# Performance work log

Hardware: AMD Instinct MI355X
Metric: run time of the kernel (lower is better)

Reference implementation:

```python
import jax, jax.numpy as jnp
from jax import lax
import numpy as np

D_COND = 48      # d_condition
K = 24           # n_bins
HID = 128        # hidden_dim
T = 10           # n_transforms
TAIL = 15.0      # tail_bound
B = 131072       # batch (contexts x samples flattened, as in sample())


def setup_inputs() -> dict:
    key = jax.random.key(0)
    ks = jax.random.split(key, 8)
    def w(k, shape, fan_in, gain=1.0):
        return (jax.random.normal(k, shape, jnp.float32) * (gain / np.sqrt(fan_in))).astype(jnp.float32)
    return {
        "z": jax.random.normal(ks[0], (B,), jnp.float32),
        "context": jax.random.normal(ks[1], (B, D_COND), jnp.float32),
        "W0": w(ks[2], (T, D_COND, HID), D_COND),
        "b0": jnp.zeros((T, HID), jnp.float32),
        "W1": w(ks[3], (T, HID, HID), HID),
        "b1": jnp.zeros((T, HID), jnp.float32),
        "W2": w(ks[4], (T, HID, HID), HID),
        "b2": jnp.zeros((T, HID), jnp.float32),
        "W3": w(ks[5], (T, HID, 3 * K + 1), HID, gain=0.1),
        "b3": jnp.zeros((T, 3 * K + 1), jnp.float32),
        "loc": jnp.float32(85.0),
        "scale": jnp.float32(5.0),
    }


def _spline_forward(x, widths, heights, derivs):
    # x: (B,); widths/heights: (B,K); derivs: (B,K+1)
    inside = (x >= -TAIL) & (x <= TAIL)
    cw = jnp.pad(jnp.cumsum(widths, -1), ((0, 0), (1, 0)), constant_values=-TAIL)   # (B,K+1)
    ch = jnp.pad(jnp.cumsum(heights, -1), ((0, 0), (1, 0)), constant_values=-TAIL)  # (B,K+1)
    # torch.searchsorted(cw[...,1:], x, right=False) == count of elems < x
    idx = jnp.clip(jnp.sum(cw[:, 1:] < x[:, None], axis=-1), 0, K - 1)
    take = lambda a, i: jnp.take_along_axis(a, i[:, None], axis=-1)[:, 0]
    w_k = take(widths, idx)
    h_k = take(heights, idx)
    cw_k = take(cw, idx)
    ch_k = take(ch, idx)
    d_k = take(derivs, idx)
    d_k1 = take(derivs, idx + 1)
    s = h_k / w_k
    xi = jnp.clip((x - cw_k) / w_k, 1e-6, 1.0 - 1e-6)
    one_m = 1.0 - xi
    numer = h_k * (s * xi * xi + d_k * xi * one_m)
    denom = s + (d_k + d_k1 - 2.0 * s) * xi * one_m
    y = ch_k + numer / denom
    dy_dxi = s * s * (d_k1 * xi * xi + 2.0 * s * xi * one_m + d_k * one_m * one_m) / (denom * denom)
    log_det = (jnp.log(jnp.maximum(dy_dxi, 1e-10))
               + jnp.log(jnp.maximum(h_k, 1e-10))
               - jnp.log(jnp.maximum(w_k, 1e-10)))
    y = jnp.where(inside, y, x)
    log_det = jnp.where(inside, log_det, 0.0)
    return y, log_det


def reference(z, context, W0, b0, W1, b1, W2, b2, W3, b3, loc, scale):
    def body(carry, p):
        zc, ld = carry
        w0, c0, w1, c1, w2, c2, w3, c3 = p
        h = jax.nn.silu(context @ w0 + c0)
        h = jax.nn.silu(h @ w1 + c1)
        h = jax.nn.silu(h @ w2 + c2)
        params = h @ w3 + c3                                   # (B, 3K+1)
        Wl, Hl, Dl = params[:, :K], params[:, K:2 * K], params[:, 2 * K:]
        widths = jax.nn.softmax(Wl, axis=-1) * (2.0 * TAIL)
        heights = jax.nn.softmax(Hl, axis=-1) * (2.0 * TAIL)
        derivs = jax.nn.softplus(Dl) + 1e-3
        y, l = _spline_forward(zc, widths, heights, derivs)
        return (y, ld + l), None

    (z_out, total_ld), _ = lax.scan(body, (z, jnp.zeros_like(z)),
                                    (W0, b0, W1, b1, W2, b2, W3, b3))
    s = jnp.maximum(scale, 0.1)
    temp_f = z_out * s + loc   # _unstandardize, as in sample()
    return temp_f, total_ld
```

## Files before the change

kernel.cpp:

```cpp
#include <hip/hip_runtime.h>
#include <hip/hip_bf16.h>

#define DCOND 48
#define KBINS 24
#define HID 128
#define TSTEPS 10
#define NPAR 73
#define TAILF 15.0f

typedef __attribute__((ext_vector_type(8))) short v8s;
typedef __attribute__((ext_vector_type(4))) float f32x4;
typedef __attribute__((ext_vector_type(4))) unsigned u32x4;

__device__ __forceinline__ short f2bf(float f) {
    __hip_bfloat16 h = __float2bfloat16(f);
    return __builtin_bit_cast(short, h);
}
__device__ __forceinline__ float bf2f(short s) {
    unsigned u = ((unsigned)(unsigned short)s) << 16;
    return __builtin_bit_cast(float, u);
}
__device__ __forceinline__ float silu_f(float v) {
    return __fdividef(v, 1.0f + __expf(-v));
}

__device__ __forceinline__ unsigned cvt_pk(float a, float b) {
    unsigned r;
    asm("v_cvt_pk_bf16_f32 %0, %1, %2" : "=v"(r) : "v"(a), "v"(b));
    return r;
}

__device__ __forceinline__ void split8(f32x4 a0, f32x4 a1, v8s& hi, v8s& lo) {
    unsigned h0 = cvt_pk(a0[0], a0[1]);
    unsigned h1 = cvt_pk(a0[2], a0[3]);
    unsigned h2 = cvt_pk(a1[0], a1[1]);
    unsigned h3 = cvt_pk(a1[2], a1[3]);
    float l0 = a0[0] - __builtin_bit_cast(float, h0 << 16);
    float l1 = a0[1] - __builtin_bit_cast(float, h0 & 0xffff0000u);
    float l2 = a0[2] - __builtin_bit_cast(float, h1 << 16);
    float l3 = a0[3] - __builtin_bit_cast(float, h1 & 0xffff0000u);
    float l4 = a1[0] - __builtin_bit_cast(float, h2 << 16);
    float l5 = a1[1] - __builtin_bit_cast(float, h2 & 0xffff0000u);
    float l6 = a1[2] - __builtin_bit_cast(float, h3 << 16);
    float l7 = a1[3] - __builtin_bit_cast(float, h3 & 0xffff0000u);
    unsigned q0 = cvt_pk(l0, l1);
    unsigned q1 = cvt_pk(l2, l3);
    unsigned q2 = cvt_pk(l4, l5);
    unsigned q3 = cvt_pk(l6, l7);
    hi = __builtin_bit_cast(v8s, (u32x4){h0, h1, h2, h3});
    lo = __builtin_bit_cast(v8s, (u32x4){q0, q1, q2, q3});
}

__global__ void prep_w(const float* __restrict__ W0, const float* __restrict__ W1,
                       const float* __restrict__ W2, const float* __restrict__ W3,
                       short* __restrict__ ws)
{
    int g = blockIdx.x * 256 + threadIdx.x;
    if (g >= TSTEPS * 51200) return;
    int t = g / 51200;
    int r = g % 51200;

    int base_e, elems, NT, Kreal, Nreal;
    const float* W;
    if (r < 8192)       { base_e = 0;     elems = 8192;  NT = 8; Kreal = 48;  Nreal = 128; W = W0 + (size_t)t * DCOND * HID; }
    else if (r < 24576) { base_e = 8192;  elems = 16384; NT = 8; Kreal = 128; Nreal = 128; W = W1 + (size_t)t * HID * HID; }
    else if (r < 40960) { base_e = 24576; elems = 16384; NT = 8; Kreal = 128; Nreal = 128; W = W2 + (size_t)t * HID * HID; }
    else                { base_e = 40960; elems = 10240; NT = 5; Kreal = 128; Nreal = 73;  W = W3 + (size_t)t * HID * NPAR; }

    int e  = r - base_e;
    int j  = e & 7;
    int ln = (e >> 3) & 63;
    int q  = e >> 9;
    int nt = q % NT, kc = q / NT;
    int k  = kc * 32 + (ln >> 4) * 8 + j;
    int n  = nt * 16 + (ln & 15);

    float v = 0.0f;
    if (k < Kreal && n < Nreal) v = W[(size_t)k * Nreal + n];
    short hi = f2bf(v);
    short lo = f2bf(v - bf2f(hi));

    size_t o = (size_t)t * 102400 + 2 * (size_t)base_e + e;
    ws[o]         = hi;
    ws[o + elems] = lo;
}

#define MBLK 128
#define NTHR 512

template<int ROUNDS>
__device__ __forceinline__ void w_issue(const short* __restrict__ g, int tid, v8s (&r)[8]) {
    #pragma unroll
    for (int i = 0; i < ROUNDS; ++i)
        r[i] = *(const v8s*)(g + tid * 8 + i * 4096);
}
template<int ROUNDS>
__device__ __forceinline__ void w_flush(short* __restrict__ lds, int tid, const v8s (&r)[8]) {
    #pragma unroll
    for (int i = 0; i < ROUNDS; ++i)
        *(v8s*)(lds + tid * 8 + i * 4096) = r[i];
}

template<int KC, int NT, int ELEMS, bool ACT, bool AREG>
__device__ __forceinline__ void layer_run(const float* __restrict__ bias, int nreal,
                                          float* __restrict__ Hlds,
                                          const short* __restrict__ Wb,
                                          int lane, int wave,
                                          const v8s* cxh, const v8s* cxl)
{
    const int arow = wave * 16 + (lane & 15);
    const int asw  = (arow & 7) << 4;
    const int kg   = (lane >> 4) * 8;

    v8s ah[KC], al[KC];
    if (AREG) {
        #pragma unroll
        for (int kc = 0; kc < KC; ++kc) { ah[kc] = cxh[kc]; al[kc] = cxl[kc]; }
    } else {
        #pragma unroll
        for (int kc = 0; kc < KC; ++kc) {
            const int kb = (kc * 32 + kg) * 4;
            f32x4 a0 = *(const f32x4*)((const char*)Hlds + arow * 512 + (kb ^ asw));
            f32x4 a1 = *(const f32x4*)((const char*)Hlds + arow * 512 + ((kb + 16) ^ asw));
            split8(a0, a1, ah[kc], al[kc]);
        }
    }

    const int crow0 = wave * 16 + (lane >> 4) * 4;
    const int ncol  = lane & 15;

    #pragma unroll
    for (int np = 0; np < NT / 2; ++np) {
        const int nt0 = np * 2, nt1 = np * 2 + 1;
        const int n0 = nt0 * 16 + ncol, n1 = nt1 * 16 + ncol;
        const float bv0 = (n0 < nreal) ? bias[n0] : 0.0f;
        const float bv1 = (n1 < nreal) ? bias[n1] : 0.0f;
        f32x4 acc0 = {bv0, bv0, bv0, bv0};
        f32x4 acc1 = {bv1, bv1, bv1, bv1};
        #pragma unroll
        for (int kc = 0; kc < KC; ++kc) {
            const short* bp0 = Wb + ((size_t)(kc * NT + nt0) * 64 + lane) * 8;
            const short* bp1 = Wb + ((size_t)(kc * NT + nt1) * 64 + lane) * 8;
            v8s bh0 = *(const v8s*)bp0;
            v8s bl0 = *(const v8s*)(bp0 + ELEMS);
            v8s bh1 = *(const v8s*)bp1;
            v8s bl1 = *(const v8s*)(bp1 + ELEMS);
            acc0 = __builtin_amdgcn_mfma_f32_16x16x32_bf16(ah[kc], bh0, acc0, 0, 0, 0);
            acc1 = __builtin_amdgcn_mfma_f32_16x16x32_bf16(ah[kc], bh1, acc1, 0, 0, 0);
            acc0 = __builtin_amdgcn_mfma_f32_16x16x32_bf16(ah[kc], bl0, acc0, 0, 0, 0);
            acc1 = __builtin_amdgcn_mfma_f32_16x16x32_bf16(ah[kc], bl1, acc1, 0, 0, 0);
            acc0 = __builtin_amdgcn_mfma_f32_16x16x32_bf16(al[kc], bh0, acc0, 0, 0, 0);
            acc1 = __builtin_amdgcn_mfma_f32_16x16x32_bf16(al[kc], bh1, acc1, 0, 0, 0);
        }
        #pragma unroll
        for (int r = 0; r < 4; ++r) {
            const int row = crow0 + r;
            const int sw  = (row & 7) << 4;
            float v0 = acc0[r], v1 = acc1[r];
            if (ACT) { v0 = silu_f(v0); v1 = silu_f(v1); }
            *(float*)((char*)Hlds + row * 512 + ((n0 * 4) ^ sw)) = v0;
            *(float*)((char*)Hlds + row * 512 + ((n1 * 4) ^ sw)) = v1;
        }
    }
    if (NT & 1) {
        const int nt = NT - 1;
        const int n0 = nt * 16 + ncol;
        const float bv0 = (n0 < nreal) ? bias[n0] : 0.0f;
        f32x4 acc0 = {bv0, bv0, bv0, bv0};
        #pragma unroll
        for (int kc = 0; kc < KC; ++kc) {
            const short* bp0 = Wb + ((size_t)(kc * NT + nt) * 64 + lane) * 8;
            v8s bh0 = *(const v8s*)bp0;
            v8s bl0 = *(const v8s*)(bp0 + ELEMS);
            acc0 = __builtin_amdgcn_mfma_f32_16x16x32_bf16(ah[kc], bh0, acc0, 0, 0, 0);
            acc0 = __builtin_amdgcn_mfma_f32_16x16x32_bf16(ah[kc], bl0, acc0, 0, 0, 0);
            acc0 = __builtin_amdgcn_mfma_f32_16x16x32_bf16(al[kc], bh0, acc0, 0, 0, 0);
        }
        #pragma unroll
        for (int r = 0; r < 4; ++r) {
            const int row = crow0 + r;
            const int sw  = (row & 7) << 4;
            float v0 = acc0[r];
            if (ACT) v0 = silu_f(v0);
            *(float*)((char*)Hlds + row * 512 + ((n0 * 4) ^ sw)) = v0;
        }
    }
}

__global__ __launch_bounds__(NTHR, 2)
void nsf_mfma(const float* __restrict__ z_g, const float* __restrict__ ctx_g,
              const float* __restrict__ b0g, const float* __restrict__ b1g,
              const float* __restrict__ b2g, const float* __restrict__ b3g,
              const float* __restrict__ locp, const float* __restrict__ sclp,
              const short* __restrict__ wsW, float* __restrict__ out, int B)
{
    __shared__ float Hlds[MBLK * 128];
    __shared__ short Wlds[32768];
    const int tid  = threadIdx.x;
    const int lane = tid & 63, wave = tid >> 6;
    const int blk  = blockIdx.x;

    v8s wreg[8];
    w_issue<4>(wsW, tid, wreg);

    v8s cxh[2], cxl[2];
    {
        const int arow = wave * 16 + (lane & 15);
        int gidr = blk * MBLK + arow;
        if (gidr > B - 1) gidr = B - 1;
        const int k0 = (lane >> 4) * 8;
        const float* cg = ctx_g + (size_t)gidr * DCOND;
        f32x4 c0 = *(const f32x4*)(cg + k0);
        f32x4 c1 = *(const f32x4*)(cg + k0 + 4);
        split8(c0, c1, cxh[0], cxl[0]);
        if ((lane >> 4) < 2) {
            f32x4 c2 = *(const f32x4*)(cg + 32 + k0);
            f32x4 c3 = *(const f32x4*)(cg + 36 + k0);
            split8(c2, c3, cxh[1], cxl[1]);
        } else {
            #pragma unroll
            for (int u = 0; u < 8; ++u) { cxh[1][u] = 0; cxl[1][u] = 0; }
        }
    }

    float x = 0.0f, ld = 0.0f;
    if (lane < 16) {
        int gid = blk * MBLK + wave * 16 + lane;
        if (gid > B - 1) gid = B - 1;
        x = z_g[gid];
    }

    #pragma unroll 1
    for (int t = 0; t < TSTEPS; ++t) {
        const short* wstep = wsW + (size_t)t * 102400;
        const short* wnext = wsW + (size_t)((t + 1) % TSTEPS) * 102400;

        w_flush<4>(Wlds, tid, wreg);
        w_issue<8>(wstep + 16384, tid, wreg);
        __syncthreads();

        layer_run<2, 8, 8192, true, true>(b0g + t * HID, HID, Hlds, Wlds,
                                          lane, wave, cxh, cxl);
        __syncthreads();

        w_flush<8>(Wlds, tid, wreg);
        w_issue<8>(wstep + 49152, tid, wreg);
        __syncthreads();

        layer_run<4, 8, 16384, true, false>(b1g + t * HID, HID, Hlds, Wlds,
                                            lane, wave, nullptr, nullptr);
        __syncthreads();

        w_flush<8>(Wlds, tid, wreg);
        w_issue<5>(wstep + 81920, tid, wreg);
        __syncthreads();

        layer_run<4, 8, 16384, true, false>(b2g + t * HID, HID, Hlds, Wlds,
                                            lane, wave, nullptr, nullptr);
        __syncthreads();

        w_flush<5>(Wlds, tid, wreg);
        w_issue<4>(wnext, tid, wreg);
        __syncthreads();

        layer_run<4, 5, 10240, false, false>(b3g + t * NPAR, NPAR, Hlds, Wlds,
                                             lane, wave, nullptr, nullptr);

        if (lane < 16) {
            const int rowS = wave * 16 + lane;
            const char* hrow = (const char*)Hlds + rowS * 512;
            const int sw = (rowS & 7) << 4;

            float pw[KBINS], ph[KBINS];
            #pragma unroll
            for (int g = 0; g < 6; ++g) {
                f32x4 vw = *(const f32x4*)(hrow + ((g * 16) ^ sw));
                f32x4 vh = *(const f32x4*)(hrow + (((g + 6) * 16) ^ sw));
                #pragma unroll
                for (int u = 0; u < 4; ++u) { pw[g * 4 + u] = vw[u]; ph[g * 4 + u] = vh[u]; }
            }
            float mw = pw[0], mh = ph[0];
            #pragma unroll
            for (int i = 1; i < KBINS; ++i) { mw = fmaxf(mw, pw[i]); mh = fmaxf(mh, ph[i]); }
            float wsum = 0.0f, hsum = 0.0f;
            #pragma unroll
            for (int i = 0; i < KBINS; ++i) {
                pw[i] = __expf(pw[i] - mw); wsum += pw[i];
                ph[i] = __expf(ph[i] - mh); hsum += ph[i];
            }
            const float wmul = __fdividef(2.0f * TAILF, wsum);
            const float hmul = __fdividef(2.0f * TAILF, hsum);

            float cw = 0.0f, ch = 0.0f;
            float cwk = -TAILF, chk = -TAILF;
            float wk = pw[0] * wmul, hk = ph[0] * hmul;
            int idx = 0;
            #pragma unroll
            for (int i = 1; i < KBINS; ++i) {
                cw += pw[i - 1] * wmul;
                ch += ph[i - 1] * hmul;
                if (cw < x) {
                    cwk = cw; chk = ch;
                    wk = pw[i] * wmul; hk = ph[i] * hmul;
                    idx = i;
                }
            }
            float d0 = *(const float*)(hrow + (((2 * KBINS + idx) * 4) ^ sw));
            float d1 = *(const float*)(hrow + (((2 * KBINS + idx + 1) * 4) ^ sw));
            const float dk  = fmaxf(d0, 0.0f) + __logf(1.0f + __expf(-fabsf(d0))) + 0.001f;
            const float dk1 = fmaxf(d1, 0.0f) + __logf(1.0f + __expf(-fabsf(d1))) + 0.001f;

            const bool inside = (x >= -TAILF) && (x <= TAILF);
            const float sr = __fdividef(hk, wk);
            float xi = __fdividef(x - cwk, wk);
            xi = fminf(fmaxf(xi, 1e-6f), 1.0f - 1e-6f);
            const float om  = 1.0f - xi;
            const float xio = xi * om;
            const float numer = hk * (sr * xi * xi + dk * xio);
            const float denom = sr + (dk + dk1 - 2.0f * sr) * xio;
            const float y = chk + __fdividef(numer, denom);
            const float dyd = __fdividef(sr * sr * (dk1 * xi * xi + 2.0f * sr * xio + dk * om * om),
                                         denom * denom);
            const float lg = __logf(fmaxf(dyd, 1e-10f)) + __logf(fmaxf(hk, 1e-10f))
                           - __logf(fmaxf(wk, 1e-10f));
            x  = inside ? y : x;
            ld += inside ? lg : 0.0f;
        }
        __syncthreads();
    }

    if (lane < 16) {
        const int gid = blk * MBLK + wave * 16 + lane;
        if (gid < B) {
            const float s = fmaxf(sclp[0], 0.1f);
            out[gid]     = fmaf(x, s, locp[0]);
            out[B + gid] = ld;
        }
    }
}

#define FBLK 256
template<int KIN, int WS, int NOUT, bool ACT>
__device__ __forceinline__ void dense_chunk(const float* __restrict__ W,
                                            const float* __restrict__ bias,
                                            int j0, const float (&hin)[KIN],
                                            float* __restrict__ sb, int tid)
{
    #pragma unroll 1
    for (int jj = 0; jj < NOUT; jj += 8) {
        const int j = j0 + jj;
        float a[8];
        #pragma unroll
        for (int u = 0; u < 8; ++u) a[u] = bias[j + u];
        #pragma unroll
        for (int k = 0; k < KIN; ++k) {
            const float* w = W + k * WS + j;
            const float hk = hin[k];
            #pragma unroll
            for (int u = 0; u < 8; ++u) a[u] = fmaf(hk, w[u], a[u]);
        }
        #pragma unroll
        for (int u = 0; u < 8; ++u) {
            float v = ACT ? silu_f(a[u]) : a[u];
            sb[(jj + u) * FBLK + tid] = v;
        }
    }
}

__global__ __launch_bounds__(FBLK, 2)
void nsf_fwd_slow(const float* __restrict__ z_g, const float* __restrict__ ctx_g,
                  const float* __restrict__ W0g, const float* __restrict__ b0g,
                  const float* __restrict__ W1g, const float* __restrict__ b1g,
                  const float* __restrict__ W2g, const float* __restrict__ b2g,
                  const float* __restrict__ W3g, const float* __restrict__ b3g,
                  const float* __restrict__ locp, const float* __restrict__ sclp,
                  float* __restrict__ out, int B)
{
    __shared__ float sbuf[64 * FBLK];
    const int tid = threadIdx.x;
    const int gid = blockIdx.x * FBLK + tid;
    if (gid >= B) return;
    float x = z_g[gid], ld = 0.0f;
    #pragma unroll 1
    for (int t = 0; t < TSTEPS; ++t) {
        asm volatile("" ::: "memory");
        const float* W0 = W0g + (size_t)t * DCOND * HID;
        const float* b0 = b0g + (size_t)t * HID;
        const float* W1 = W1g + (size_t)t * HID * HID;
        const float* b1 = b1g + (size_t)t * HID;
        const float* W2 = W2g + (size_t)t * HID * HID;
        const float* b2 = b2g + (size_t)t * HID;
        const float* W3 = W3g + (size_t)t * HID * NPAR;
        const float* b3 = b3g + (size_t)t * NPAR;
        float ctx[DCOND];
        #pragma unroll
        for (int k = 0; k < DCOND; ++k) ctx[k] = ctx_g[(size_t)gid * DCOND + k];
        float h[HID];
        dense_chunk<DCOND, HID, 64, true>(W0, b0, 0, ctx, sbuf, tid);
        #pragma unroll
        for (int j = 0; j < 64; ++j) h[j] = sbuf[j * FBLK + tid];
        dense_chunk<DCOND, HID, 64, true>(W0, b0, 64, ctx, sbuf, tid);
        #pragma unroll
        for (int j = 0; j < 64; ++j) h[64 + j] = sbuf[j * FBLK + tid];
        #pragma unroll 1
        for (int l = 0; l < 2; ++l) {
            const float* W  = (l == 0) ? W1 : W2;
            const float* bb = (l == 0) ? b1 : b2;
            float hlo[64];
            dense_chunk<HID, HID, 64, true>(W, bb, 0, h, sbuf, tid);
            #pragma unroll
            for (int j = 0; j < 64; ++j) hlo[j] = sbuf[j * FBLK + tid];
            dense_chunk<HID, HID, 64, true>(W, bb, 64, h, sbuf, tid);
            #pragma unroll
            for (int j = 0; j < 64; ++j) h[64 + j] = sbuf[j * FBLK + tid];
            #pragma unroll
            for (int j = 0; j < 64; ++j) h[j] = hlo[j];
        }
        float p[NPAR];
        dense_chunk<HID, NPAR, 64, false>(W3, b3, 0, h, sbuf, tid);
        #pragma unroll
        for (int j = 0; j < 64; ++j) p[j] = sbuf[j * FBLK + tid];
        dense_chunk<HID, NPAR, 8, false>(W3, b3, 64, h, sbuf, tid);
        #pragma unroll
        for (int j = 0; j < 8; ++j) p[64 + j] = sbuf[j * FBLK + tid];
        {
            float a = b3[72];
            #pragma unroll
            for (int k = 0; k < HID; ++k) a = fmaf(h[k], W3[k * NPAR + 72], a);
            p[72] = a;
        }
        float mw = p[0];
        #pragma unroll
        for (int i = 1; i < KBINS; ++i) mw = fmaxf(mw, p[i]);
        float we[KBINS]; float wsum = 0.0f;
        #pragma unroll
        for (int i = 0; i < KBINS; ++i) { we[i] = __expf(p[i] - mw); wsum += we[i]; }
        const float wmul = __fdividef(2.0f * TAILF, wsum);
        float mh = p[KBINS];
        #pragma unroll
        for (int i = 1; i < KBINS; ++i) mh = fmaxf(mh, p[KBINS + i]);
        float he[KBINS]; float hsum = 0.0f;
        #pragma unroll
        for (int i = 0; i < KBINS; ++i) { he[i] = __expf(p[KBINS + i] - mh); hsum += he[i]; }
        const float hmul = __fdividef(2.0f * TAILF, hsum);
        float dvv[KBINS + 1];
        #pragma unroll
        for (int i = 0; i <= KBINS; ++i) {
            float xd = p[2 * KBINS + i];
            dvv[i] = fmaxf(xd, 0.0f) + __logf(1.0f + __expf(-fabsf(xd))) + 0.001f;
        }
        float cw = 0.0f, ch = 0.0f, cwk = -TAILF, chk = -TAILF;
        float wk = we[0] * wmul, hk = he[0] * hmul, dk = dvv[0], dk1 = dvv[1];
        #pragma unroll
        for (int i = 1; i < KBINS; ++i) {
            cw += we[i - 1] * wmul;
            ch += he[i - 1] * hmul;
            if (cw < x) {
                cwk = cw; chk = ch;
                wk = we[i] * wmul; hk = he[i] * hmul;
                dk = dvv[i]; dk1 = dvv[i + 1];
            }
        }
        const bool inside = (x >= -TAILF) && (x <= TAILF);
        const float sr = __fdividef(hk, wk);
        float xi = __fdividef(x - cwk, wk);
        xi = fminf(fmaxf(xi, 1e-6f), 1.0f - 1e-6f);
        const float om  = 1.0f - xi;
        const float xio = xi * om;
        const float numer = hk * (sr * xi * xi + dk * xio);
        const float denom = sr + (dk + dk1 - 2.0f * sr) * xio;
        const float y = chk + __fdividef(numer, denom);
        const float dyd = __fdividef(sr * sr * (dk1 * xi * xi + 2.0f * sr * xio + dk * om * om),
                                     denom * denom);
        const float lg = __logf(fmaxf(dyd, 1e-10f)) + __logf(fmaxf(hk, 1e-10f))
                       - __logf(fmaxf(wk, 1e-10f));
        x  = inside ? y : x;
        ld += inside ? lg : 0.0f;
    }
    const float s = fmaxf(sclp[0], 0.1f);
    out[gid]     = fmaf(x, s, locp[0]);
    out[B + gid] = ld;
}

extern "C" void kernel_launch(void* const* d_in, const int* in_sizes, int n_in,
                              void* d_out, int out_size, void* d_ws, size_t ws_size,
                              hipStream_t stream) {
    const float* z    = (const float*)d_in[0];
    const float* ctx  = (const float*)d_in[1];
    const float* W0   = (const float*)d_in[2];
    const float* b0   = (const float*)d_in[3];
    const float* W1   = (const float*)d_in[4];
    const float* b1   = (const float*)d_in[5];
    const float* W2   = (const float*)d_in[6];
    const float* b2   = (const float*)d_in[7];
    const float* W3   = (const float*)d_in[8];
    const float* b3   = (const float*)d_in[9];
    const float* loc  = (const float*)d_in[10];
    const float* scl  = (const float*)d_in[11];
    float* out = (float*)d_out;
    const int B = in_sizes[0];

    const size_t ws_need = (size_t)TSTEPS * 102400 * sizeof(short);
    if (ws_size < ws_need) {
        const int nblk = (B + FBLK - 1) / FBLK;
        hipLaunchKernelGGL(nsf_fwd_slow, dim3(nblk), dim3(FBLK), 0, stream,
                           z, ctx, W0, b0, W1, b1, W2, b2, W3, b3, loc, scl, out, B);
        return;
    }

    short* ws = (short*)d_ws;
    const int prep_total = TSTEPS * 51200;
    hipLaunchKernelGGL(prep_w, dim3((prep_total + 255) / 256), dim3(256), 0, stream,
                       W0, W1, W2, W3, ws);

    const int nblk = (B + MBLK - 1) / MBLK;
    hipLaunchKernelGGL(nsf_mfma, dim3(nblk), dim3(NTHR), 0, stream,
                       z, ctx, b0, b1, b2, b3, loc, scl, ws, out, B);
}
```

Measured before the change: 627.7 us.

## Read MFMA weight fragments directly from global memory and drop block-level LDS staging

Removes the LDS weight staging buffer and register-prefetch pipeline, so each wave loads its bf16 hi/lo weight fragments straight from global memory (expected to hit in L1/L2). Each wave now owns a private 16-row slice of the activation buffer, which lets every __syncthreads in the time loop go away. The block shrinks to 256 threads and 64 rows, with occupancy raised to 3 blocks per CU. This trades LDS capacity and barrier stalls for more global or cache weight traffic per wave and loses the explicit overlap of weight loads with compute.

```diff
diff --git a/kernel.cpp b/kernel.cpp
--- a/kernel.cpp
+++ b/kernel.cpp
@@ -85,30 +85,19 @@
     ws[o + elems] = lo;
 }
 
-#define MBLK 128
-#define NTHR 512
-
-template<int ROUNDS>
-__device__ __forceinline__ void w_issue(const short* __restrict__ g, int tid, v8s (&r)[8]) {
-    #pragma unroll
-    for (int i = 0; i < ROUNDS; ++i)
-        r[i] = *(const v8s*)(g + tid * 8 + i * 4096);
-}
-template<int ROUNDS>
-__device__ __forceinline__ void w_flush(short* __restrict__ lds, int tid, const v8s (&r)[8]) {
-    #pragma unroll
-    for (int i = 0; i < ROUNDS; ++i)
-        *(v8s*)(lds + tid * 8 + i * 4096) = r[i];
-}
+#define WAVEM 16
+#define NWAVE 4
+#define MBLK  (WAVEM * NWAVE)
+#define NTHR  256
 
 template<int KC, int NT, int ELEMS, bool ACT, bool AREG>
 __device__ __forceinline__ void layer_run(const float* __restrict__ bias, int nreal,
-                                          float* __restrict__ Hlds,
-                                          const short* __restrict__ Wb,
-                                          int lane, int wave,
+                                          char* __restrict__ hb,
+                                          const short* __restrict__ Wg,
+                                          int lane,
                                           const v8s* cxh, const v8s* cxl)
 {
-    const int arow = wave * 16 + (lane & 15);
+    const int arow = lane & 15;
     const int asw  = (arow & 7) << 4;
     const int kg   = (lane >> 4) * 8;
 
@@ -120,14 +109,15 @@
         #pragma unroll
         for (int kc = 0; kc < KC; ++kc) {
             const int kb = (kc * 32 + kg) * 4;
-            f32x4 a0 = *(const f32x4*)((const char*)Hlds + arow * 512 + (kb ^ asw));
-            f32x4 a1 = *(const f32x4*)((const char*)Hlds + arow * 512 + ((kb + 16) ^ asw));
+            f32x4 a0 = *(const f32x4*)(hb + arow * 512 + (kb ^ asw));
+            f32x4 a1 = *(const f32x4*)(hb + arow * 512 + ((kb + 16) ^ asw));
             split8(a0, a1, ah[kc], al[kc]);
         }
     }
 
-    const int crow0 = wave * 16 + (lane >> 4) * 4;
+    const int crow0 = (lane >> 4) * 4;
     const int ncol  = lane & 15;
+    const short* bbase = Wg + lane * 8;
 
     #pragma unroll
     for (int np = 0; np < NT / 2; ++np) {
@@ -139,8 +129,8 @@
         f32x4 acc1 = {bv1, bv1, bv1, bv1};
         #pragma unroll
         for (int kc = 0; kc < KC; ++kc) {
-            const short* bp0 = Wb + ((size_t)(kc * NT + nt0) * 64 + lane) * 8;
-            const short* bp1 = Wb + ((size_t)(kc * NT + nt1) * 64 + lane) * 8;
+            const short* bp0 = bbase + (size_t)(kc * NT + nt0) * 512;
+            const short* bp1 = bbase + (size_t)(kc * NT + nt1) * 512;
             v8s bh0 = *(const v8s*)bp0;
             v8s bl0 = *(const v8s*)(bp0 + ELEMS);
             v8s bh1 = *(const v8s*)bp1;
@@ -158,8 +148,8 @@
             const int sw  = (row & 7) << 4;
             float v0 = acc0[r], v1 = acc1[r];
             if (ACT) { v0 = silu_f(v0); v1 = silu_f(v1); }
-            *(float*)((char*)Hlds + row * 512 + ((n0 * 4) ^ sw)) = v0;
-            *(float*)((char*)Hlds + row * 512 + ((n1 * 4) ^ sw)) = v1;
+            *(float*)(hb + row * 512 + ((n0 * 4) ^ sw)) = v0;
+            *(float*)(hb + row * 512 + ((n1 * 4) ^ sw)) = v1;
         }
     }
     if (NT & 1) {
@@ -169,7 +159,7 @@
         f32x4 acc0 = {bv0, bv0, bv0, bv0};
         #pragma unroll
         for (int kc = 0; kc < KC; ++kc) {
-            const short* bp0 = Wb + ((size_t)(kc * NT + nt) * 64 + lane) * 8;
+            const short* bp0 = bbase + (size_t)(kc * NT + nt) * 512;
             v8s bh0 = *(const v8s*)bp0;
             v8s bl0 = *(const v8s*)(bp0 + ELEMS);
             acc0 = __builtin_amdgcn_mfma_f32_16x16x32_bf16(ah[kc], bh0, acc0, 0, 0, 0);
@@ -182,12 +172,12 @@
             const int sw  = (row & 7) << 4;
             float v0 = acc0[r];
             if (ACT) v0 = silu_f(v0);
-            *(float*)((char*)Hlds + row * 512 + ((n0 * 4) ^ sw)) = v0;
-        }
-    }
-}
-
-__global__ __launch_bounds__(NTHR, 2)
+            *(float*)(hb + row * 512 + ((n0 * 4) ^ sw)) = v0;
+        }
+    }
+}
+
+__global__ __launch_bounds__(NTHR, 3)
 void nsf_mfma(const float* __restrict__ z_g, const float* __restrict__ ctx_g,
               const float* __restrict__ b0g, const float* __restrict__ b1g,
               const float* __restrict__ b2g, const float* __restrict__ b3g,
@@ -195,18 +185,15 @@
               const short* __restrict__ wsW, float* __restrict__ out, int B)
 {
     __shared__ float Hlds[MBLK * 128];
-    __shared__ short Wlds[32768];
     const int tid  = threadIdx.x;
     const int lane = tid & 63, wave = tid >> 6;
     const int blk  = blockIdx.x;
-
-    v8s wreg[8];
-    w_issue<4>(wsW, tid, wreg);
+    char* hb = (char*)(Hlds + wave * WAVEM * 128);
 
     v8s cxh[2], cxl[2];
     {
-        const int arow = wave * 16 + (lane & 15);
-        int gidr = blk * MBLK + arow;
+        const int arow = lane & 15;
+        int gidr = blk * MBLK + wave * WAVEM + arow;
         if (gidr > B - 1) gidr = B - 1;
         const int k0 = (lane >> 4) * 8;
         const float* cg = ctx_g + (size_t)gidr * DCOND;
@@ -225,7 +212,7 @@
 
     float x = 0.0f, ld = 0.0f;
     if (lane < 16) {
-        int gid = blk * MBLK + wave * 16 + lane;
+        int gid = blk * MBLK + wave * WAVEM + lane;
         if (gid > B - 1) gid = B - 1;
         x = z_g[gid];
     }
@@ -233,43 +220,19 @@
     #pragma unroll 1
     for (int t = 0; t < TSTEPS; ++t) {
         const short* wstep = wsW + (size_t)t * 102400;
-        const short* wnext = wsW + (size_t)((t + 1) % TSTEPS) * 102400;
-
-        w_flush<4>(Wlds, tid, wreg);
-        w_issue<8>(wstep + 16384, tid, wreg);
-        __syncthreads();
-
-        layer_run<2, 8, 8192, true, true>(b0g + t * HID, HID, Hlds, Wlds,
-                                          lane, wave, cxh, cxl);
-        __syncthreads();
-
-        w_flush<8>(Wlds, tid, wreg);
-        w_issue<8>(wstep + 49152, tid, wreg);
-        __syncthreads();
-
-        layer_run<4, 8, 16384, true, false>(b1g + t * HID, HID, Hlds, Wlds,
-                                            lane, wave, nullptr, nullptr);
-        __syncthreads();
-
-        w_flush<8>(Wlds, tid, wreg);
-        w_issue<5>(wstep + 81920, tid, wreg);
-        __syncthreads();
-
-        layer_run<4, 8, 16384, true, false>(b2g + t * HID, HID, Hlds, Wlds,
-                                            lane, wave, nullptr, nullptr);
-        __syncthreads();
-
-        w_flush<5>(Wlds, tid, wreg);
-        w_issue<4>(wnext, tid, wreg);
-        __syncthreads();
-
-        layer_run<4, 5, 10240, false, false>(b3g + t * NPAR, NPAR, Hlds, Wlds,
-                                             lane, wave, nullptr, nullptr);
+
+        layer_run<2, 8, 8192, true, true>(b0g + t * HID, HID, hb,
+                                          wstep, lane, cxh, cxl);
+        layer_run<4, 8, 16384, true, false>(b1g + t * HID, HID, hb,
+                                            wstep + 16384, lane, nullptr, nullptr);
+        layer_run<4, 8, 16384, true, false>(b2g + t * HID, HID, hb,
+                                            wstep + 49152, lane, nullptr, nullptr);
+        layer_run<4, 5, 10240, false, false>(b3g + t * NPAR, NPAR, hb,
+                                             wstep + 81920, lane, nullptr, nullptr);
 
         if (lane < 16) {
-            const int rowS = wave * 16 + lane;
-            const char* hrow = (const char*)Hlds + rowS * 512;
-            const int sw = (rowS & 7) << 4;
+            const char* hrow = hb + lane * 512;
+            const int sw = (lane & 7) << 4;
 
             float pw[KBINS], ph[KBINS];
             #pragma unroll
@@ -326,11 +289,10 @@
             x  = inside ? y : x;
             ld += inside ? lg : 0.0f;
         }
-        __syncthreads();
     }
 
     if (lane < 16) {
-        const int gid = blk * MBLK + wave * 16 + lane;
+        const int gid = blk * MBLK + wave * WAVEM + lane;
         if (gid < B) {
             const float s = fmaxf(sclp[0], 0.1f);
             out[gid]     = fmaf(x, s, locp[0]);
```

Result: slower. 909.3 us (+44.9%).

## Tile MLP waves as 32 rows by half columns to reuse B-fragments

Applied to the files above, without the earlier changes.

Each pair of waves now shares a 32-row slab of the hidden activations, and each wave computes half of the output columns for both 16-row M tiles. Every weight fragment loaded from LDS is therefore reused across two MFMA row tiles, which halves LDS weight reads per MFMA. The final layer's 5 column tiles are split 3/2 between the paired waves, and the trailing barrier moves so that it sits before the spline epilogue. In exchange, A-fragment register usage doubles, which may pressure occupancy, and the last layer is load-imbalanced.

```diff
diff --git a/kernel.cpp b/kernel.cpp
--- a/kernel.cpp
+++ b/kernel.cpp
@@ -101,88 +101,110 @@
         *(v8s*)(lds + tid * 8 + i * 4096) = r[i];
 }
 
-template<int KC, int NT, int ELEMS, bool ACT, bool AREG>
+template<int KC, int NTN, int NTOT, int ELEMS, bool ACT, bool AREG>
 __device__ __forceinline__ void layer_run(const float* __restrict__ bias, int nreal,
-                                          float* __restrict__ Hlds,
-                                          const short* __restrict__ Wb,
-                                          int lane, int wave,
+                                          char* __restrict__ hb,
+                                          const short* __restrict__ Wbh,
+                                          int lane, int nb0,
                                           const v8s* cxh, const v8s* cxl)
 {
-    const int arow = wave * 16 + (lane & 15);
-    const int asw  = (arow & 7) << 4;
-    const int kg   = (lane >> 4) * 8;
-
-    v8s ah[KC], al[KC];
-    if (AREG) {
-        #pragma unroll
-        for (int kc = 0; kc < KC; ++kc) { ah[kc] = cxh[kc]; al[kc] = cxl[kc]; }
-    } else {
+    const int kg = (lane >> 4) * 8;
+
+    v8s ah[2][KC], al[2][KC];
+    #pragma unroll
+    for (int mt = 0; mt < 2; ++mt) {
+        const int arow = mt * 16 + (lane & 15);
+        const int asw  = (arow & 7) << 4;
         #pragma unroll
         for (int kc = 0; kc < KC; ++kc) {
-            const int kb = (kc * 32 + kg) * 4;
-            f32x4 a0 = *(const f32x4*)((const char*)Hlds + arow * 512 + (kb ^ asw));
-            f32x4 a1 = *(const f32x4*)((const char*)Hlds + arow * 512 + ((kb + 16) ^ asw));
-            split8(a0, a1, ah[kc], al[kc]);
-        }
-    }
-
-    const int crow0 = wave * 16 + (lane >> 4) * 4;
+            if (AREG) {
+                ah[mt][kc] = cxh[mt * KC + kc];
+                al[mt][kc] = cxl[mt * KC + kc];
+            } else {
+                const int kb = (kc * 32 + kg) * 4;
+                f32x4 a0 = *(const f32x4*)(hb + arow * 512 + (kb ^ asw));
+                f32x4 a1 = *(const f32x4*)(hb + arow * 512 + ((kb + 16) ^ asw));
+                split8(a0, a1, ah[mt][kc], al[mt][kc]);
+            }
+        }
+    }
+
     const int ncol  = lane & 15;
+    const int crow  = (lane >> 4) * 4;
+    const short* bbase = Wbh + lane * 8;
 
     #pragma unroll
-    for (int np = 0; np < NT / 2; ++np) {
-        const int nt0 = np * 2, nt1 = np * 2 + 1;
-        const int n0 = nt0 * 16 + ncol, n1 = nt1 * 16 + ncol;
+    for (int np = 0; np < NTN / 2; ++np) {
+        const int n0 = nb0 + np * 32 + ncol;
+        const int n1 = n0 + 16;
         const float bv0 = (n0 < nreal) ? bias[n0] : 0.0f;
         const float bv1 = (n1 < nreal) ? bias[n1] : 0.0f;
-        f32x4 acc0 = {bv0, bv0, bv0, bv0};
-        f32x4 acc1 = {bv1, bv1, bv1, bv1};
+        f32x4 a00 = {bv0, bv0, bv0, bv0}, a01 = {bv1, bv1, bv1, bv1};
+        f32x4 a10 = {bv0, bv0, bv0, bv0}, a11 = {bv1, bv1, bv1, bv1};
         #pragma unroll
         for (int kc = 0; kc < KC; ++kc) {
-            const short* bp0 = Wb + ((size_t)(kc * NT + nt0) * 64 + lane) * 8;
-            const short* bp1 = Wb + ((size_t)(kc * NT + nt1) * 64 + lane) * 8;
+            const short* bp0 = bbase + (kc * NTOT + np * 2) * 512;
+            const short* bp1 = bp0 + 512;
             v8s bh0 = *(const v8s*)bp0;
             v8s bl0 = *(const v8s*)(bp0 + ELEMS);
             v8s bh1 = *(const v8s*)bp1;
             v8s bl1 = *(const v8s*)(bp1 + ELEMS);
-            acc0 = __builtin_amdgcn_mfma_f32_16x16x32_bf16(ah[kc], bh0, acc0, 0, 0, 0);
-            acc1 = __builtin_amdgcn_mfma_f32_16x16x32_bf16(ah[kc], bh1, acc1, 0, 0, 0);
-            acc0 = __builtin_amdgcn_mfma_f32_16x16x32_bf16(ah[kc], bl0, acc0, 0, 0, 0);
-            acc1 = __builtin_amdgcn_mfma_f32_16x16x32_bf16(ah[kc], bl1, acc1, 0, 0, 0);
-            acc0 = __builtin_amdgcn_mfma_f32_16x16x32_bf16(al[kc], bh0, acc0, 0, 0, 0);
-            acc1 = __builtin_amdgcn_mfma_f32_16x16x32_bf16(al[kc], bh1, acc1, 0, 0, 0);
-        }
-        #pragma unroll
-        for (int r = 0; r < 4; ++r) {
-            const int row = crow0 + r;
-            const int sw  = (row & 7) << 4;
-            float v0 = acc0[r], v1 = acc1[r];
-            if (ACT) { v0 = silu_f(v0); v1 = silu_f(v1); }
-            *(float*)((char*)Hlds + row * 512 + ((n0 * 4) ^ sw)) = v0;
-            *(float*)((char*)Hlds + row * 512 + ((n1 * 4) ^ sw)) = v1;
-        }
-    }
-    if (NT & 1) {
-        const int nt = NT - 1;
-        const int n0 = nt * 16 + ncol;
+            a00 = __builtin_amdgcn_mfma_f32_16x16x32_bf16(ah[0][kc], bh0, a00, 0, 0, 0);
+            a01 = __builtin_amdgcn_mfma_f32_16x16x32_bf16(ah[0][kc], bh1, a01, 0, 0, 0);
+            a10 = __builtin_amdgcn_mfma_f32_16x16x32_bf16(ah[1][kc], bh0, a10, 0, 0, 0);
+            a11 = __builtin_amdgcn_mfma_f32_16x16x32_bf16(ah[1][kc], bh1, a11, 0, 0, 0);
+            a00 = __builtin_amdgcn_mfma_f32_16x16x32_bf16(ah[0][kc], bl0, a00, 0, 0, 0);
+            a01 = __builtin_amdgcn_mfma_f32_16x16x32_bf16(ah[0][kc], bl1, a01, 0, 0, 0);
+            a10 = __builtin_amdgcn_mfma_f32_16x16x32_bf16(ah[1][kc], bl0, a10, 0, 0, 0);
+            a11 = __builtin_amdgcn_mfma_f32_16x16x32_bf16(ah[1][kc], bl1, a11, 0, 0, 0);
+            a00 = __builtin_amdgcn_mfma_f32_16x16x32_bf16(al[0][kc], bh0, a00, 0, 0, 0);
+            a01 = __builtin_amdgcn_mfma_f32_16x16x32_bf16(al[0][kc], bh1, a01, 0, 0, 0);
+            a10 = __builtin_amdgcn_mfma_f32_16x16x32_bf16(al[1][kc], bh0, a10, 0, 0, 0);
+            a11 = __builtin_amdgcn_mfma_f32_16x16x32_bf16(al[1][kc], bh1, a11, 0, 0, 0);
+        }
+        #pragma unroll
+        for (int mt = 0; mt < 2; ++mt) {
+            const f32x4 c0 = mt ? a10 : a00;
+            const f32x4 c1 = mt ? a11 : a01;
+            #pragma unroll
+            for (int r = 0; r < 4; ++r) {
+                const int row = mt * 16 + crow + r;
+                const int sw  = (row & 7) << 4;
+                float v0 = c0[r], v1 = c1[r];
+                if (ACT) { v0 = silu_f(v0); v1 = silu_f(v1); }
+                *(float*)(hb + row * 512 + ((n0 * 4) ^ sw)) = v0;
+                *(float*)(hb + row * 512 + ((n1 * 4) ^ sw)) = v1;
+            }
+        }
+    }
+    if (NTN & 1) {
+        const int n0 = nb0 + (NTN - 1) * 16 + ncol;
         const float bv0 = (n0 < nreal) ? bias[n0] : 0.0f;
-        f32x4 acc0 = {bv0, bv0, bv0, bv0};
+        f32x4 a00 = {bv0, bv0, bv0, bv0};
+        f32x4 a10 = {bv0, bv0, bv0, bv0};
         #pragma unroll
         for (int kc = 0; kc < KC; ++kc) {
-            const short* bp0 = Wb + ((size_t)(kc * NT + nt) * 64 + lane) * 8;
+            const short* bp0 = bbase + (kc * NTOT + NTN - 1) * 512;
             v8s bh0 = *(const v8s*)bp0;
             v8s bl0 = *(const v8s*)(bp0 + ELEMS);
-            acc0 = __builtin_amdgcn_mfma_f32_16x16x32_bf16(ah[kc], bh0, acc0, 0, 0, 0);
-            acc0 = __builtin_amdgcn_mfma_f32_16x16x32_bf16(ah[kc], bl0, acc0, 0, 0, 0);
-            acc0 = __builtin_amdgcn_mfma_f32_16x16x32_bf16(al[kc], bh0, acc0, 0, 0, 0);
-        }
-        #pragma unroll
-        for (int r = 0; r < 4; ++r) {
-            const int row = crow0 + r;
-            const int sw  = (row & 7) << 4;
-            float v0 = acc0[r];
-            if (ACT) v0 = silu_f(v0);
-            *(float*)((char*)Hlds + row * 512 + ((n0 * 4) ^ sw)) = v0;
+            a00 = __builtin_amdgcn_mfma_f32_16x16x32_bf16(ah[0][kc], bh0, a00, 0, 0, 0);
+            a10 = __builtin_amdgcn_mfma_f32_16x16x32_bf16(ah[1][kc], bh0, a10, 0, 0, 0);
+            a00 = __builtin_amdgcn_mfma_f32_16x16x32_bf16(ah[0][kc], bl0, a00, 0, 0, 0);
+            a10 = __builtin_amdgcn_mfma_f32_16x16x32_bf16(ah[1][kc], bl0, a10, 0, 0, 0);
+            a00 = __builtin_amdgcn_mfma_f32_16x16x32_bf16(al[0][kc], bh0, a00, 0, 0, 0);
+            a10 = __builtin_amdgcn_mfma_f32_16x16x32_bf16(al[1][kc], bh0, a10, 0, 0, 0);
+        }
+        #pragma unroll
+        for (int mt = 0; mt < 2; ++mt) {
+            const f32x4 c0 = mt ? a10 : a00;
+            #pragma unroll
+            for (int r = 0; r < 4; ++r) {
+                const int row = mt * 16 + crow + r;
+                const int sw  = (row & 7) << 4;
+                float v0 = c0[r];
+                if (ACT) v0 = silu_f(v0);
+                *(float*)(hb + row * 512 + ((n0 * 4) ^ sw)) = v0;
+            }
         }
     }
 }
@@ -198,34 +220,38 @@
     __shared__ short Wlds[32768];
     const int tid  = threadIdx.x;
     const int lane = tid & 63, wave = tid >> 6;
+    const int p    = wave >> 1, h = wave & 1;
     const int blk  = blockIdx.x;
+    char* hb = (char*)Hlds + p * 32 * 512;
 
     v8s wreg[8];
     w_issue<4>(wsW, tid, wreg);
 
-    v8s cxh[2], cxl[2];
+    v8s cxh[4], cxl[4];
     {
-        const int arow = wave * 16 + (lane & 15);
-        int gidr = blk * MBLK + arow;
-        if (gidr > B - 1) gidr = B - 1;
         const int k0 = (lane >> 4) * 8;
-        const float* cg = ctx_g + (size_t)gidr * DCOND;
-        f32x4 c0 = *(const f32x4*)(cg + k0);
-        f32x4 c1 = *(const f32x4*)(cg + k0 + 4);
-        split8(c0, c1, cxh[0], cxl[0]);
-        if ((lane >> 4) < 2) {
-            f32x4 c2 = *(const f32x4*)(cg + 32 + k0);
-            f32x4 c3 = *(const f32x4*)(cg + 36 + k0);
-            split8(c2, c3, cxh[1], cxl[1]);
-        } else {
-            #pragma unroll
-            for (int u = 0; u < 8; ++u) { cxh[1][u] = 0; cxl[1][u] = 0; }
+        #pragma unroll
+        for (int mt = 0; mt < 2; ++mt) {
+            int gidr = blk * MBLK + p * 32 + mt * 16 + (lane & 15);
+            if (gidr > B - 1) gidr = B - 1;
+            const float* cg = ctx_g + (size_t)gidr * DCOND;
+            f32x4 c0 = *(const f32x4*)(cg + k0);
+            f32x4 c1 = *(const f32x4*)(cg + k0 + 4);
+            split8(c0, c1, cxh[mt * 2 + 0], cxl[mt * 2 + 0]);
+            if ((lane >> 4) < 2) {
+                f32x4 c2 = *(const f32x4*)(cg + 32 + k0);
+                f32x4 c3 = *(const f32x4*)(cg + 36 + k0);
+                split8(c2, c3, cxh[mt * 2 + 1], cxl[mt * 2 + 1]);
+            } else {
+                #pragma unroll
+                for (int u = 0; u < 8; ++u) { cxh[mt * 2 + 1][u] = 0; cxl[mt * 2 + 1][u] = 0; }
+            }
         }
     }
 
     float x = 0.0f, ld = 0.0f;
     if (lane < 16) {
-        int gid = blk * MBLK + wave * 16 + lane;
+        int gid = blk * MBLK + p * 32 + h * 16 + lane;
         if (gid > B - 1) gid = B - 1;
         x = z_g[gid];
     }
@@ -239,37 +265,42 @@
         w_issue<8>(wstep + 16384, tid, wreg);
         __syncthreads();
 
-        layer_run<2, 8, 8192, true, true>(b0g + t * HID, HID, Hlds, Wlds,
-                                          lane, wave, cxh, cxl);
+        layer_run<2, 4, 8, 8192, true, true>(b0g + t * HID, HID, hb,
+                                             Wlds + h * 2048, lane, h * 64, cxh, cxl);
         __syncthreads();
 
         w_flush<8>(Wlds, tid, wreg);
         w_issue<8>(wstep + 49152, tid, wreg);
         __syncthreads();
 
-        layer_run<4, 8, 16384, true, false>(b1g + t * HID, HID, Hlds, Wlds,
-                                            lane, wave, nullptr, nullptr);
+        layer_run<4, 4, 8, 16384, true, false>(b1g + t * HID, HID, hb,
+                                               Wlds + h * 2048, lane, h * 64, nullptr, nullptr);
         __syncthreads();
 
         w_flush<8>(Wlds, tid, wreg);
         w_issue<5>(wstep + 81920, tid, wreg);
         __syncthreads();
 
-        layer_run<4, 8, 16384, true, false>(b2g + t * HID, HID, Hlds, Wlds,
-                                            lane, wave, nullptr, nullptr);
+        layer_run<4, 4, 8, 16384, true, false>(b2g + t * HID, HID, hb,
+                                               Wlds + h * 2048, lane, h * 64, nullptr, nullptr);
         __syncthreads();
 
         w_flush<5>(Wlds, tid, wreg);
         w_issue<4>(wnext, tid, wreg);
         __syncthreads();
 
-        layer_run<4, 5, 10240, false, false>(b3g + t * NPAR, NPAR, Hlds, Wlds,
-                                             lane, wave, nullptr, nullptr);
+        if (h == 0)
+            layer_run<4, 3, 5, 10240, false, false>(b3g + t * NPAR, NPAR, hb,
+                                                    Wlds, lane, 0, nullptr, nullptr);
+        else
+            layer_run<4, 2, 5, 10240, false, false>(b3g + t * NPAR, NPAR, hb,
+                                                    Wlds + 1536, lane, 48, nullptr, nullptr);
+        __syncthreads();
 
         if (lane < 16) {
-            const int rowS = wave * 16 + lane;
-            const char* hrow = (const char*)Hlds + rowS * 512;
-            const int sw = (rowS & 7) << 4;
+            const int srow = h * 16 + lane;
+            const char* hrow = hb + srow * 512;
+            const int sw = (srow & 7) << 4;
 
             float pw[KBINS], ph[KBINS];
             #pragma unroll
@@ -326,11 +357,10 @@
             x  = inside ? y : x;
             ld += inside ? lg : 0.0f;
         }
-        __syncthreads();
     }
 
     if (lane < 16) {
-        const int gid = blk * MBLK + wave * 16 + lane;
+        const int gid = blk * MBLK + p * 32 + h * 16 + lane;
         if (gid < B) {
             const float s = fmaxf(sclp[0], 0.1f);
             out[gid]     = fmaf(x, s, locp[0]);
```

Result: slower. 761.1 us (+21.2%).
